# Performance work log

Measured on AMD Instinct MI355X. Metric: run time of the kernel, lower is better.

The kernel has to match this reference:

```python
import math
import jax, jax.numpy as jnp
import numpy as np

B, N_PER, FEAT, EMB, HEADS, E = 64, 512, 128, 128, 3, 131072
NEG = -1e9


def _gat(x, src, dst, emask, W, a_src, a_dst, bias):
    # PyG GATConv (concat heads, add_self_loops=True, negative_slope=0.2, eval mode -> no dropout)
    n = x.shape[0]
    H, C = a_src.shape
    h = (x @ W).reshape(n, H, C)                      # [n,H,C]
    e_src = (h * a_src[None]).sum(-1)                 # [n,H]
    e_dst = (h * a_dst[None]).sum(-1)                 # [n,H]
    loop = jnp.arange(n)
    s = jnp.concatenate([src, loop])
    d = jnp.concatenate([dst, loop])
    m = jnp.concatenate([emask, jnp.ones((n,), dtype=bool)])
    logit = jax.nn.leaky_relu(e_src[s] + e_dst[d], negative_slope=0.2)  # [E+n,H]
    logit = jnp.where(m[:, None], logit, NEG)
    mx = jax.ops.segment_max(logit, d, num_segments=n)
    ex = jnp.exp(logit - mx[d]) * m[:, None].astype(logit.dtype)
    den = jax.ops.segment_sum(ex, d, num_segments=n)
    alpha = ex / (den[d] + 1e-16)                     # edge-softmax over incoming edges
    out = jax.ops.segment_sum(alpha[:, :, None] * h[s], d, num_segments=n)
    return out.reshape(n, H * C) + bias


def _topk_pool(x, src, dst, emask, ratio, w):
    # PyG TopKPooling: score = tanh(x.w/||w||), keep ceil(ratio*n) per graph, gate kept x by score
    n = x.shape[0]
    per = n // B
    score = jnp.tanh((x @ w) / jnp.linalg.norm(w))    # [n]
    k = int(math.ceil(ratio * per))
    _, idx = jax.lax.top_k(score.reshape(B, per), k)  # [B,k]
    perm = (idx + (jnp.arange(B) * per)[:, None]).reshape(-1)
    xn = x[perm] * score[perm][:, None]
    newid = jnp.full((n,), -1, dtype=jnp.int32).at[perm].set(jnp.arange(B * k, dtype=jnp.int32))
    ns, nd = newid[src], newid[dst]
    valid = emask & (ns >= 0) & (nd >= 0)
    src = jnp.where(valid, ns, 0)
    dst = jnp.where(valid, nd, 0)
    batch = jnp.repeat(jnp.arange(B, dtype=jnp.int32), k)
    return xn, src, dst, valid, batch


def _gpool(x, batch):
    # cat([global_max_pool, global_mean_pool])
    mx = jax.ops.segment_max(x, batch, num_segments=B)
    sm = jax.ops.segment_sum(x, batch, num_segments=B)
    cnt = jax.ops.segment_sum(jnp.ones((x.shape[0], 1), x.dtype), batch, num_segments=B)
    return jnp.concatenate([mx, sm / cnt], axis=1)


def _forward(x, edge_attr, edge_index, batch_index, params):
    (W1, as1, ad1, b1, Wh1, bh1, pw1,
     W2, as2, ad2, b2, Wh2, bh2, pw2,
     W3, as3, ad3, b3, Wh3, bh3, pw3,
     Wl1, bl1, Wl2, bl2) = params
    src, dst = edge_index[0], edge_index[1]
    emask = jnp.ones((src.shape[0],), dtype=bool)

    h = _gat(x, src, dst, emask, W1, as1, ad1, b1)
    h = jax.nn.relu(h @ Wh1 + bh1)
    h, src, dst, emask, batch = _topk_pool(h, src, dst, emask, 0.8, pw1)
    x1 = _gpool(h, batch)

    h = _gat(h, src, dst, emask, W2, as2, ad2, b2)
    h = jax.nn.relu(h @ Wh2 + bh2)
    h, src, dst, emask, batch = _topk_pool(h, src, dst, emask, 0.5, pw2)
    x2 = _gpool(h, batch)

    h = _gat(h, src, dst, emask, W3, as3, ad3, b3)
    h = jax.nn.relu(h @ Wh3 + bh3)
    h, src, dst, emask, batch = _topk_pool(h, src, dst, emask, 0.2, pw3)
    x3 = _gpool(h, batch)

    z = x1 + x2 + x3
    z = jax.nn.relu(z @ Wl1 + bl1)
    # F.dropout p=0.8 skipped (eval mode)
    return z @ Wl2 + bl2


def setup_inputs() -> dict:
    key = jax.random.key(0)
    ks = jax.random.split(key, 32)
    e_per = E // B
    e = jax.random.randint(ks[0], (2, B, e_per), 0, N_PER) + (jnp.arange(B) * N_PER)[None, :, None]
    edge_index = e.reshape(2, E).astype(jnp.int32)
    inp = {
        'x': jax.random.normal(ks[1], (B * N_PER, FEAT), dtype=jnp.float32),
        'edge_attr': jnp.zeros((E, 1), dtype=jnp.float32),
        'edge_index': edge_index,
        'batch_index': jnp.repeat(jnp.arange(B, dtype=jnp.int32), N_PER),
    }
    def rn(k, shape, s=0.1):
        return jax.random.normal(k, shape, dtype=jnp.float32) * s
    names = ['W1','as1','ad1','b1','Wh1','bh1','pw1',
             'W2','as2','ad2','b2','Wh2','bh2','pw2',
             'W3','as3','ad3','b3','Wh3','bh3','pw3',
             'Wl1','bl1','Wl2','bl2']
    shapes = [(FEAT, HEADS*EMB), (HEADS, EMB), (HEADS, EMB), (HEADS*EMB,), (HEADS*EMB, EMB), (EMB,), (EMB,),
              (EMB, HEADS*EMB), (HEADS, EMB), (HEADS, EMB), (HEADS*EMB,), (HEADS*EMB, EMB), (EMB,), (EMB,),
              (EMB, HEADS*EMB), (HEADS, EMB), (HEADS, EMB), (HEADS*EMB,), (HEADS*EMB, EMB), (EMB,), (EMB,),
              (2*EMB, 512), (512,), (512, 256), (256,)]
    for i, (nm, sh) in enumerate(zip(names, shapes)):
        inp[nm] = rn(ks[2 + i], sh)
    return inp


def reference(x, edge_attr, edge_index, batch_index,
              W1, as1, ad1, b1, Wh1, bh1, pw1,
              W2, as2, ad2, b2, Wh2, bh2, pw2,
              W3, as3, ad3, b3, Wh3, bh3, pw3,
              Wl1, bl1, Wl2, bl2):
    params = (W1, as1, ad1, b1, Wh1, bh1, pw1,
              W2, as2, ad2, b2, Wh2, bh2, pw2,
              W3, as3, ad3, b3, Wh3, bh3, pw3,
              Wl1, bl1, Wl2, bl2)
    return _forward(x, edge_attr, edge_index, batch_index, params)
```

## Files before the change

### kernel.cpp

```cpp
#include <hip/hip_runtime.h>
#include <cfloat>

static __device__ __forceinline__ float lrelu(float v) { return v >= 0.f ? v : 0.2f * v; }

typedef __attribute__((ext_vector_type(8))) short bf16x8;
typedef __attribute__((ext_vector_type(8))) unsigned short ushort8;
typedef __attribute__((ext_vector_type(4))) float f32x4;

__device__ __forceinline__ unsigned short f2bf(float x) {
    unsigned u = __float_as_uint(x);
    u += 0x7FFF + ((u >> 16) & 1);
    return (unsigned short)(u >> 16);
}
__device__ __forceinline__ float bf2f(unsigned short h) {
    return __uint_as_float(((unsigned)h) << 16);
}

struct SegT { const float* s; unsigned short* dh; unsigned short* dl; int rows, cols, tr; };
struct Segs { SegT seg[7]; int cum[8]; };

__global__ __launch_bounds__(256) void split_k(Segs S, int total)
{
    int idx = blockIdx.x * 256 + threadIdx.x;
    if (idx >= total) return;
    int si = 0;
    while (idx >= S.cum[si + 1]) si++;
    int o = idx - S.cum[si];
    SegT g = S.seg[si];
    float v = g.s[o];
    unsigned short h = f2bf(v);
    unsigned short l = f2bf(v - bf2f(h));
    int di = o;
    if (g.tr) { int r = o / g.cols, c = o - r * g.cols; di = c * g.rows + r; }
    g.dh[di] = h;
    g.dl[di] = l;
}

struct WaArgs { const float* W[3]; const float* as_[3]; const float* ad_[3]; const float* pw[3]; };

__global__ __launch_bounds__(256) void wa_k(WaArgs a, float* __restrict__ wab, float* __restrict__ rn)
{
    int wid = blockIdx.x * 4 + (threadIdx.x >> 6);
    int lane = threadIdx.x & 63;
    if (wid < 2304) {
        int l = wid / 768, r = wid - l * 768;
        int j = r >> 7, kk = r & 127;
        int hh = j % 3;
        const float* av = (j < 3 ? a.as_[l] : a.ad_[l]) + hh * 128;
        const float* Wp = a.W[l] + (size_t)kk * 384 + hh * 128;
        float p = Wp[lane] * av[lane] + Wp[lane + 64] * av[lane + 64];
#pragma unroll
        for (int o = 32; o > 0; o >>= 1) p += __shfl_down(p, o);
        if (lane == 0) wab[l * 768 + j * 128 + kk] = p;
    } else if (wid < 2307) {
        int l = wid - 2304;
        const float* pw = a.pw[l];
        float v0 = pw[lane], v1 = pw[lane + 64];
        float p = v0 * v0 + v1 * v1;
#pragma unroll
        for (int o = 32; o > 0; o >>= 1) p += __shfl_down(p, o);
        if (lane == 0) rn[l] = 1.f / sqrtf(p);
    }
}

__global__ __launch_bounds__(256) void esd_k(const float* __restrict__ X,
                                             const float* __restrict__ wab,
                                             float* __restrict__ es, float* __restrict__ ed, int n)
{
    int wid = (int)((blockIdx.x * 256 + threadIdx.x) >> 6);
    int lane = threadIdx.x & 63;
    if (wid >= n) return;
    const float* xp = X + (size_t)wid * 128;
    float x0 = xp[lane], x1 = xp[lane + 64];
    float p[6];
#pragma unroll
    for (int j = 0; j < 6; j++)
        p[j] = x0 * wab[j * 128 + lane] + x1 * wab[j * 128 + 64 + lane];
#pragma unroll
    for (int o = 32; o > 0; o >>= 1)
#pragma unroll
        for (int j = 0; j < 6; j++) p[j] += __shfl_down(p[j], o);
    if (lane == 0) {
#pragma unroll
        for (int h = 0; h < 3; h++) { es[(size_t)wid * 3 + h] = p[h]; ed[(size_t)wid * 3 + h] = p[h + 3]; }
    }
}

__global__ __launch_bounds__(256) void gemm_bf2_k(const unsigned short* __restrict__ AH,
                                                  const unsigned short* __restrict__ AL,
                                                  const unsigned short* __restrict__ BTH,
                                                  const unsigned short* __restrict__ BTL,
                                                  const float* __restrict__ bias,
                                                  float* __restrict__ C,
                                                  int M, int K, int N, int relu,
                                                  const float* __restrict__ pwv,
                                                  const float* __restrict__ rnormp,
                                                  float* __restrict__ scv)
{
    __shared__ unsigned short sAH[64 * 32], sAL[64 * 32];
    __shared__ unsigned short sBH[128 * 32], sBL[128 * 32];
    __shared__ float sred[2][64];
    const int tid  = threadIdx.x;
    const int lane = tid & 63;
    const int wave = tid >> 6;
    const int wr = (wave >> 1) * 32;
    const int wc = (wave & 1) * 64;
    const int row0 = blockIdx.x * 64, col0 = blockIdx.y * 128;

    f32x4 acc[2][4];
#pragma unroll
    for (int i = 0; i < 2; i++)
#pragma unroll
        for (int j = 0; j < 4; j++) acc[i][j] = (f32x4){0.f, 0.f, 0.f, 0.f};

    const int a_r = tid >> 2;
    const int a_c = tid & 3;
    const int a_slot = a_r * 32 + ((a_c ^ ((a_r ^ (a_r >> 2)) & 3)) << 3);
    const unsigned short* ApH = AH + (size_t)(row0 + a_r) * K + a_c * 8;
    const unsigned short* ApL = AL + (size_t)(row0 + a_r) * K + a_c * 8;

    const int b_c = tid >> 1;
    const int b_h = (tid & 1) * 2;
    const int b_sw = (b_c ^ (b_c >> 2)) & 3;
    const unsigned short* BpH = BTH + (size_t)(col0 + b_c) * K + b_h * 8;
    const unsigned short* BpL = BTL + (size_t)(col0 + b_c) * K + b_h * 8;

    const int l15 = lane & 15;
    const int kc  = lane >> 4;

    for (int k0 = 0; k0 < K; k0 += 32) {
        ushort8 vah = *reinterpret_cast<const ushort8*>(ApH + k0);
        ushort8 val = *reinterpret_cast<const ushort8*>(ApL + k0);
        ushort8 vb[4];
        vb[0] = *reinterpret_cast<const ushort8*>(BpH + k0);
        vb[1] = *reinterpret_cast<const ushort8*>(BpH + k0 + 8);
        vb[2] = *reinterpret_cast<const ushort8*>(BpL + k0);
        vb[3] = *reinterpret_cast<const ushort8*>(BpL + k0 + 8);

        __syncthreads();

        *reinterpret_cast<ushort8*>(&sAH[a_slot]) = vah;
        *reinterpret_cast<ushort8*>(&sAL[a_slot]) = val;
        {
            int s0 = b_c * 32 + (((b_h + 0) ^ b_sw) << 3);
            int s1 = b_c * 32 + (((b_h + 1) ^ b_sw) << 3);
            *reinterpret_cast<ushort8*>(&sBH[s0]) = vb[0];
            *reinterpret_cast<ushort8*>(&sBH[s1]) = vb[1];
            *reinterpret_cast<ushort8*>(&sBL[s0]) = vb[2];
            *reinterpret_cast<ushort8*>(&sBL[s1]) = vb[3];
        }
        __syncthreads();

        bf16x8 aH[2], aL[2], bH[4], bL[4];
#pragma unroll
        for (int fi = 0; fi < 2; fi++) {
            int r = wr + fi * 16 + l15;
            int sidx = r * 32 + ((kc ^ ((r ^ (r >> 2)) & 3)) << 3);
            aH[fi] = *reinterpret_cast<const bf16x8*>(&sAH[sidx]);
            aL[fi] = *reinterpret_cast<const bf16x8*>(&sAL[sidx]);
        }
#pragma unroll
        for (int fj = 0; fj < 4; fj++) {
            int c = wc + fj * 16 + l15;
            int sidx = c * 32 + ((kc ^ ((c ^ (c >> 2)) & 3)) << 3);
            bH[fj] = *reinterpret_cast<const bf16x8*>(&sBH[sidx]);
            bL[fj] = *reinterpret_cast<const bf16x8*>(&sBL[sidx]);
        }
#pragma unroll
        for (int fi = 0; fi < 2; fi++)
#pragma unroll
            for (int fj = 0; fj < 4; fj++) {
                acc[fi][fj] = __builtin_amdgcn_mfma_f32_16x16x32_bf16(aH[fi], bH[fj], acc[fi][fj], 0, 0, 0);
                acc[fi][fj] = __builtin_amdgcn_mfma_f32_16x16x32_bf16(aH[fi], bL[fj], acc[fi][fj], 0, 0, 0);
                acc[fi][fj] = __builtin_amdgcn_mfma_f32_16x16x32_bf16(aL[fi], bH[fj], acc[fi][fj], 0, 0, 0);
            }
    }

    float pwl[4];
    if (scv) {
#pragma unroll
        for (int fj = 0; fj < 4; fj++) pwl[fj] = pwv[wc + fj * 16 + l15];
    }
    float pd[2][4] = {{0.f,0.f,0.f,0.f},{0.f,0.f,0.f,0.f}};
#pragma unroll
    for (int fi = 0; fi < 2; fi++) {
        int rbase = row0 + wr + fi * 16 + (lane >> 4) * 4;
#pragma unroll
        for (int q = 0; q < 4; q++) {
            int r = rbase + q;
#pragma unroll
            for (int fj = 0; fj < 4; fj++) {
                int c = col0 + wc + fj * 16 + l15;
                float v = acc[fi][fj][q];
                if (bias) v += bias[c];
                if (relu) v = fmaxf(v, 0.f);
                C[(size_t)r * N + c] = v;
                if (scv) pd[fi][q] += v * pwl[fj];
            }
        }
    }
    if (scv) {
        float rn0 = rnormp[0];
#pragma unroll
        for (int fi = 0; fi < 2; fi++)
#pragma unroll
            for (int q = 0; q < 4; q++) {
                float s = pd[fi][q];
                s += __shfl_xor(s, 1);
                s += __shfl_xor(s, 2);
                s += __shfl_xor(s, 4);
                s += __shfl_xor(s, 8);
                if (l15 == 0) sred[wc >> 6][wr + fi * 16 + (lane >> 4) * 4 + q] = s;
            }
        __syncthreads();
        if (tid < 64)
            scv[row0 + tid] = tanhf((sred[0][tid] + sred[1][tid]) * rn0);
    }
}

__global__ __launch_bounds__(256) void gemm_small_k(const float* __restrict__ A,
                                                    const float* __restrict__ B,
                                                    const float* __restrict__ bias,
                                                    float* __restrict__ C,
                                                    int M, int K, int N, int relu)
{
    int idx = blockIdx.x * 256 + threadIdx.x;
    if (idx >= M * N) return;
    int r = idx / N, c = idx - r * N;
    const float* ap = A + (size_t)r * K;
    const float* bp = B + c;
    float s = 0.f;
#pragma unroll 8
    for (int k = 0; k < K; k++) s += ap[k] * bp[(size_t)k * N];
    if (bias) s += bias[c];
    if (relu) s = fmaxf(s, 0.f);
    C[idx] = s;
}

__global__ __launch_bounds__(256) void csr_k(const int* __restrict__ src,
                                             const int* __restrict__ dst,
                                             const int* __restrict__ valid,
                                             const float* __restrict__ es,
                                             const float* __restrict__ ed,
                                             int* __restrict__ csr,
                                             int* __restrict__ beg,
                                             int* __restrict__ end,
                                             float* __restrict__ wmx,
                                             float* __restrict__ winv,
                                             float* __restrict__ wself,
                                             int per)
{
    __shared__ int sdeg[512];
    __shared__ int soff[512];
    __shared__ float ses[1536];
    __shared__ float sed[1536];
    const int g = blockIdx.x;
    const int t = threadIdx.x;
    const int bn = g * per;
    const int be = g * 2048;
    for (int i = t; i < 512; i += 256) sdeg[i] = 0;
    for (int i = t; i < per * 3; i += 256) {
        ses[i] = es[(size_t)bn * 3 + i];
        sed[i] = ed[(size_t)bn * 3 + i];
    }
    __syncthreads();
#pragma unroll
    for (int j = 0; j < 8; j++) {
        int e = be + j * 256 + t;
        if (!valid || valid[e]) atomicAdd(&sdeg[dst[e] - bn], 1);
    }
    __syncthreads();
    const int i0 = t, i1 = t + 256;
    soff[i0] = sdeg[i0]; soff[i1] = sdeg[i1];
    __syncthreads();
    for (int d = 1; d < 512; d <<= 1) {
        int a0 = (i0 >= d) ? soff[i0 - d] : 0;
        int a1 = (i1 >= d) ? soff[i1 - d] : 0;
        __syncthreads();
        soff[i0] += a0; soff[i1] += a1;
        __syncthreads();
    }
    int excl0 = 0, excl1 = 0;
    if (i0 < per) { int dg = sdeg[i0]; excl0 = soff[i0] - dg; beg[bn + i0] = be + excl0; end[bn + i0] = be + excl0 + dg; }
    if (i1 < per) { int dg = sdeg[i1]; excl1 = soff[i1] - dg; beg[bn + i1] = be + excl1; end[bn + i1] = be + excl1 + dg; }
    __syncthreads();
    if (i0 < per) { soff[i0] = excl0; sdeg[i0] = excl0; }
    if (i1 < per) { soff[i1] = excl1; sdeg[i1] = excl1; }
    __syncthreads();
#pragma unroll
    for (int j = 0; j < 8; j++) {
        int e = be + j * 256 + t;
        if (!valid || valid[e]) {
            int p = atomicAdd(&sdeg[dst[e] - bn], 1);
            csr[be + p] = e;
        }
    }
    __syncthreads();
    for (int i = t; i < per; i += 256) {
        float edv[3], m[3], den[3], selfl[3];
#pragma unroll
        for (int h = 0; h < 3; h++) {
            edv[h] = sed[i * 3 + h];
            selfl[h] = lrelu(ses[i * 3 + h] + edv[h]);
            m[h] = selfl[h];
            den[h] = 1.f;
        }
        const int pb = soff[i], pe = sdeg[i];
        for (int p = pb; p < pe; p++) {
            int e = csr[be + p];
            int sl = src[e] - bn;
#pragma unroll
            for (int h = 0; h < 3; h++) {
                float l = lrelu(ses[sl * 3 + h] + edv[h]);
                if (l <= m[h]) den[h] += __expf(l - m[h]);
                else { den[h] = den[h] * __expf(m[h] - l) + 1.f; m[h] = l; }
            }
        }
#pragma unroll
        for (int h = 0; h < 3; h++) {
            float inv = 1.f / (den[h] + 1e-16f);
            wmx[(size_t)(bn + i) * 3 + h] = m[h];
            winv[(size_t)(bn + i) * 3 + h] = inv;
            wself[(size_t)(bn + i) * 3 + h] = __expf(selfl[h] - m[h]) * inv;
        }
    }
}

__global__ __launch_bounds__(256) void agg2_k(const float* __restrict__ H,
                                              const float* __restrict__ es,
                                              const float* __restrict__ ed,
                                              const float* __restrict__ wmx,
                                              const float* __restrict__ winv,
                                              const float* __restrict__ wself,
                                              const int* __restrict__ beg,
                                              const int* __restrict__ end,
                                              const int* __restrict__ csr,
                                              const int* __restrict__ srcArr,
                                              const float* __restrict__ bias,
                                              unsigned short* __restrict__ outH,
                                              unsigned short* __restrict__ outL, int n)
{
    int nwg = gridDim.x;
    int bid = blockIdx.x;
    int swz = (bid & 7) * (nwg >> 3) + (bid >> 3);
    int wid = swz * 4 + (int)(threadIdx.x >> 6);
    int lane = threadIdx.x & 63;
    if (wid >= n) return;
    const int d = wid;
    float edv[3], mxv[3], ivv[3], wsf[3];
#pragma unroll
    for (int h = 0; h < 3; h++) {
        edv[h] = ed[(size_t)d * 3 + h];
        mxv[h] = wmx[(size_t)d * 3 + h];
        ivv[h] = winv[(size_t)d * 3 + h];
        wsf[h] = wself[(size_t)d * 3 + h];
    }
    float acc[6];
    const float* hp = H + (size_t)d * 384;
#pragma unroll
    for (int j = 0; j < 6; j++) acc[j] = wsf[j >> 1] * hp[lane + 64 * j];
    const int pb = beg[d], pe = end[d];
    for (int p = pb; p < pe; p++) {
        int eg = csr[p];
        int s = srcArr[eg];
        float w[3];
#pragma unroll
        for (int h = 0; h < 3; h++) {
            float l = lrelu(es[(size_t)s * 3 + h] + edv[h]);
            w[h] = __expf(l - mxv[h]) * ivv[h];
        }
        const float* sp = H + (size_t)s * 384;
        acc[0] += w[0] * sp[lane];
        acc[1] += w[0] * sp[lane + 64];
        acc[2] += w[1] * sp[lane + 128];
        acc[3] += w[1] * sp[lane + 192];
        acc[4] += w[2] * sp[lane + 256];
        acc[5] += w[2] * sp[lane + 320];
    }
#pragma unroll
    for (int j = 0; j < 6; j++) {
        float v = acc[j] + bias[lane + 64 * j];
        unsigned short h = f2bf(v);
        outH[(size_t)d * 384 + lane + 64 * j] = h;
        outL[(size_t)d * 384 + lane + 64 * j] = f2bf(v - bf2f(h));
    }
}

__global__ __launch_bounds__(512) void select_k(const float* __restrict__ sc,
                                                int per, int k,
                                                int* __restrict__ perm, float* __restrict__ ps,
                                                int* __restrict__ newid)
{
    __shared__ float s[512];
    __shared__ int id[512];
    const int b = blockIdx.x;
    const int t = threadIdx.x;
    const int P = blockDim.x;
    if (t < per) { s[t] = sc[(size_t)b * per + t]; id[t] = t; }
    else         { s[t] = -FLT_MAX; id[t] = per + t; }
    __syncthreads();
    for (int kk = 2; kk <= P; kk <<= 1)
        for (int j = kk >> 1; j > 0; j >>= 1) {
            int ixj = t ^ j;
            if (ixj > t) {
                float a = s[t], bq = s[ixj];
                int ia = id[t], ib = id[ixj];
                bool aBefore = (a > bq) || (a == bq && ia < ib);
                bool up = ((t & kk) == 0);
                if (up ? !aBefore : aBefore) { s[t] = bq; s[ixj] = a; id[t] = ib; id[ixj] = ia; }
            }
            __syncthreads();
        }
    if (t < k) {
        int og = b * per + id[t];
        int ng = b * k + t;
        perm[ng] = og;
        ps[ng] = s[t];
        newid[og] = ng;
    } else if (t < per) {
        newid[b * per + id[t]] = -1;
    }
}

__global__ __launch_bounds__(256) void gate_k(const float* __restrict__ H,
                                              const int* __restrict__ perm,
                                              const float* __restrict__ ps,
                                              float* __restrict__ X,
                                              unsigned short* __restrict__ XH,
                                              unsigned short* __restrict__ XL, int nNew)
{
    int wid = (int)((blockIdx.x * 256 + threadIdx.x) >> 6);
    int lane = threadIdx.x & 63;
    if (wid >= nNew) return;
    int o = perm[wid];
    float g = ps[wid];
    float v0 = H[(size_t)o * 128 + lane] * g;
    float v1 = H[(size_t)o * 128 + 64 + lane] * g;
    X[(size_t)wid * 128 + lane] = v0;
    X[(size_t)wid * 128 + 64 + lane] = v1;
    unsigned short h0 = f2bf(v0), h1 = f2bf(v1);
    XH[(size_t)wid * 128 + lane] = h0;
    XH[(size_t)wid * 128 + 64 + lane] = h1;
    XL[(size_t)wid * 128 + lane] = f2bf(v0 - bf2f(h0));
    XL[(size_t)wid * 128 + 64 + lane] = f2bf(v1 - bf2f(h1));
}

__global__ __launch_bounds__(256) void remap_k(const int* __restrict__ s_old,
                                               const int* __restrict__ d_old,
                                               const int* __restrict__ v_old,
                                               const int* __restrict__ newid,
                                               int* __restrict__ s_new, int* __restrict__ d_new,
                                               int* __restrict__ v_new, int E)
{
    int e = blockIdx.x * 256 + threadIdx.x;
    if (e >= E) return;
    int v = v_old ? v_old[e] : 1;
    int ns = -1, nd = -1;
    if (v) { ns = newid[s_old[e]]; nd = newid[d_old[e]]; }
    int ok = (v && ns >= 0 && nd >= 0) ? 1 : 0;
    s_new[e] = ok ? ns : 0;
    d_new[e] = ok ? nd : 0;
    v_new[e] = ok;
}

__global__ __launch_bounds__(1024) void gpool_k(const float* __restrict__ X,
                                                float* __restrict__ z, int k, int first)
{
    __shared__ float smx[8][128];
    __shared__ float ssm[8][128];
    const int b = blockIdx.x;
    const int col = threadIdx.x & 127;
    const int rg = threadIdx.x >> 7;
    const float* xp = X + (size_t)b * k * 128 + col;
    float mx = -FLT_MAX, sm = 0.f;
    int r = rg;
#pragma unroll 4
    for (; r + 32 <= k; r += 32) {
        float v0 = xp[(size_t)(r + 0)  * 128];
        float v1 = xp[(size_t)(r + 8)  * 128];
        float v2 = xp[(size_t)(r + 16) * 128];
        float v3 = xp[(size_t)(r + 24) * 128];
        mx = fmaxf(fmaxf(fmaxf(mx, v0), fmaxf(v1, v2)), v3);
        sm += v0 + v1 + v2 + v3;
    }
    for (; r < k; r += 8) {
        float v = xp[(size_t)r * 128];
        mx = fmaxf(mx, v);
        sm += v;
    }
    smx[rg][col] = mx;
    ssm[rg][col] = sm;
    __syncthreads();
    if (rg == 0) {
#pragma unroll
        for (int i = 1; i < 8; i++) { mx = fmaxf(mx, smx[i][col]); sm += ssm[i][col]; }
        if (first) {
            z[b * 256 + col] = mx;
            z[b * 256 + 128 + col] = sm / (float)k;
        } else {
            z[b * 256 + col] += mx;
            z[b * 256 + 128 + col] += sm / (float)k;
        }
    }
}

extern "C" void kernel_launch(void* const* d_in, const int* in_sizes, int n_in,
                              void* d_out, int out_size, void* d_ws, size_t ws_size,
                              hipStream_t stream)
{
    (void)in_sizes; (void)n_in; (void)out_size; (void)ws_size;

    const float* x   = (const float*)d_in[0];
    const int*   ei  = (const int*)d_in[2];
    const float* W1  = (const float*)d_in[4];
    const float* as1 = (const float*)d_in[5];
    const float* ad1 = (const float*)d_in[6];
    const float* b1  = (const float*)d_in[7];
    const float* Wh1 = (const float*)d_in[8];
    const float* bh1 = (const float*)d_in[9];
    const float* pw1 = (const float*)d_in[10];
    const float* W2  = (const float*)d_in[11];
    const float* as2 = (const float*)d_in[12];
    const float* ad2 = (const float*)d_in[13];
    const float* b2  = (const float*)d_in[14];
    const float* Wh2 = (const float*)d_in[15];
    const float* bh2 = (const float*)d_in[16];
    const float* pw2 = (const float*)d_in[17];
    const float* W3  = (const float*)d_in[18];
    const float* as3 = (const float*)d_in[19];
    const float* ad3 = (const float*)d_in[20];
    const float* b3  = (const float*)d_in[21];
    const float* Wh3 = (const float*)d_in[22];
    const float* bh3 = (const float*)d_in[23];
    const float* pw3 = (const float*)d_in[24];
    const float* Wl1 = (const float*)d_in[25];
    const float* bl1 = (const float*)d_in[26];
    const float* Wl2 = (const float*)d_in[27];
    const float* bl2 = (const float*)d_in[28];
    float* out = (float*)d_out;

    const int E = 131072;
    const int n1 = 32768, per1 = 512, k1 = 410;
    const int n2 = 64 * k1, per2 = k1, k2 = 205;
    const int n3 = 64 * k2, per3 = k2, k3 = 41;
    const int n4 = 64 * k3;

    char* wsb = (char*)d_ws;
    size_t off = 0;
    auto alloc = [&](size_t bytes) -> void* {
        void* p = wsb + off;
        off += (bytes + 255) & ~(size_t)255;
        return p;
    };
    float* A    = (float*)alloc((size_t)n1 * 384 * 4);
    unsigned short* BfH = (unsigned short*)alloc((size_t)n1 * 384 * 2);
    unsigned short* BfL = (unsigned short*)alloc((size_t)n1 * 384 * 2);
    unsigned short* X0H = (unsigned short*)alloc((size_t)n1 * 128 * 2);
    unsigned short* X0L = (unsigned short*)alloc((size_t)n1 * 128 * 2);
    unsigned short* XaH = (unsigned short*)alloc((size_t)n2 * 128 * 2);
    unsigned short* XaL = (unsigned short*)alloc((size_t)n2 * 128 * 2);
    unsigned short* WT[6], *WTl[6];
    for (int i = 0; i < 6; i++) {
        WT[i]  = (unsigned short*)alloc((size_t)49152 * 2);
        WTl[i] = (unsigned short*)alloc((size_t)49152 * 2);
    }
    float* ES   = (float*)alloc((size_t)n1 * 3 * 4);
    float* ED   = (float*)alloc((size_t)n1 * 3 * 4);
    float* SC   = (float*)alloc((size_t)n1 * 4);
    int*   CSR  = (int*)alloc((size_t)E * 4);
    int*   BEG  = (int*)alloc((size_t)n1 * 4);
    int*   END  = (int*)alloc((size_t)n1 * 4);
    int*   SRCA = (int*)alloc((size_t)E * 4);
    int*   DSTA = (int*)alloc((size_t)E * 4);
    int*   VALA = (int*)alloc((size_t)E * 4);
    int*   SRCB = (int*)alloc((size_t)E * 4);
    int*   DSTB = (int*)alloc((size_t)E * 4);
    int*   VALB = (int*)alloc((size_t)E * 4);
    float* X1   = (float*)alloc((size_t)n2 * 128 * 4);
    float* X2   = (float*)alloc((size_t)n3 * 128 * 4);
    float* X3   = (float*)alloc((size_t)n4 * 128 * 4);
    int*   PERM = (int*)alloc((size_t)n2 * 4);
    float* PSC  = (float*)alloc((size_t)n2 * 4);
    int*   NEWID= (int*)alloc((size_t)n1 * 4);
    float* WMX  = (float*)alloc((size_t)n1 * 3 * 4);
    float* WINV = (float*)alloc((size_t)n1 * 3 * 4);
    float* WSELF= (float*)alloc((size_t)n1 * 3 * 4);
    float* WAB  = (float*)alloc((size_t)2304 * 4);
    float* RN   = (float*)alloc((size_t)4 * 4);
    float* Z    = (float*)alloc((size_t)64 * 256 * 4);
    float* ZH   = (float*)alloc((size_t)64 * 512 * 4);

    {
        Segs S;
        const float* srcs[7] = {x, W1, Wh1, W2, Wh2, W3, Wh3};
        unsigned short* dh[7] = {X0H, WT[0], WT[1], WT[2], WT[3], WT[4], WT[5]};
        unsigned short* dl[7] = {X0L, WTl[0], WTl[1], WTl[2], WTl[3], WTl[4], WTl[5]};
        int rows[7] = {n1, 128, 384, 128, 384, 128, 384};
        int cols[7] = {128, 384, 128, 384, 128, 384, 128};
        int trs[7]  = {0, 1, 1, 1, 1, 1, 1};
        int cum = 0;
        for (int i = 0; i < 7; i++) {
            S.seg[i] = SegT{srcs[i], dh[i], dl[i], rows[i], cols[i], trs[i]};
            S.cum[i] = cum;
            cum += rows[i] * cols[i];
        }
        S.cum[7] = cum;
        split_k<<<(cum + 255) / 256, 256, 0, stream>>>(S, cum);

        WaArgs wa;
        wa.W[0] = W1;  wa.W[1] = W2;  wa.W[2] = W3;
        wa.as_[0] = as1; wa.as_[1] = as2; wa.as_[2] = as3;
        wa.ad_[0] = ad1; wa.ad_[1] = ad2; wa.ad_[2] = ad3;
        wa.pw[0] = pw1; wa.pw[1] = pw2; wa.pw[2] = pw3;
        wa_k<<<(2307 + 3) / 4, 256, 0, stream>>>(wa, WAB, RN);
    }

    auto layer = [&](const float* Xf, const unsigned short* xh, const unsigned short* xl,
                     int n, int per, int kk, int lidx,
                     const int* src, const int* dst, const int* val,
                     const unsigned short* wt, const unsigned short* wtl, const float* bb,
                     const unsigned short* wht, const unsigned short* whtl, const float* bh,
                     const float* pw,
                     float* Xn, unsigned short* XnH, unsigned short* XnL, int nNew,
                     int* srcN, int* dstN, int* valN)
    {
        esd_k<<<n / 4, 256, 0, stream>>>(Xf, WAB + lidx * 768, ES, ED, n);
        gemm_bf2_k<<<dim3(n / 64, 3), 256, 0, stream>>>(xh, xl, wt, wtl, nullptr, A, n, 128, 384, 0,
                                                        nullptr, nullptr, nullptr);
        csr_k<<<64, 256, 0, stream>>>(src, dst, val, ES, ED, CSR, BEG, END, WMX, WINV, WSELF, per);
        agg2_k<<<n / 4, 256, 0, stream>>>(A, ES, ED, WMX, WINV, WSELF, BEG, END, CSR, src, bb, BfH, BfL, n);
        gemm_bf2_k<<<dim3(n / 64, 1), 256, 0, stream>>>(BfH, BfL, wht, whtl, bh, A, n, 384, 128, 1,
                                                        pw, RN + lidx, SC);
        int P2 = 1;
        while (P2 < per) P2 <<= 1;
        select_k<<<64, P2, 0, stream>>>(SC, per, kk, PERM, PSC, NEWID);
        gate_k<<<nNew / 4, 256, 0, stream>>>(A, PERM, PSC, Xn, XnH, XnL, nNew);
        if (srcN) remap_k<<<E / 256, 256, 0, stream>>>(src, dst, val, NEWID, srcN, dstN, valN, E);
        gpool_k<<<64, 1024, 0, stream>>>(Xn, Z, kk, lidx == 0 ? 1 : 0);
    };

    layer(x,  X0H, X0L, n1, per1, k1, 0, ei,   ei + E, nullptr,
          WT[0], WTl[0], b1, WT[1], WTl[1], bh1, pw1,
          X1, XaH, XaL, n2, SRCA, DSTA, VALA);
    layer(X1, XaH, XaL, n2, per2, k2, 1, SRCA, DSTA, VALA,
          WT[2], WTl[2], b2, WT[3], WTl[3], bh2, pw2,
          X2, XaH, XaL, n3, SRCB, DSTB, VALB);
    layer(X2, XaH, XaL, n3, per3, k3, 2, SRCB, DSTB, VALB,
          WT[4], WTl[4], b3, WT[5], WTl[5], bh3, pw3,
          X3, XaH, XaL, n4, nullptr, nullptr, nullptr);

    gemm_small_k<<<(64 * 512 + 255) / 256, 256, 0, stream>>>(Z,  Wl1, bl1, ZH,  64, 256, 512, 1);
    gemm_small_k<<<(64 * 256 + 255) / 256, 256, 0, stream>>>(ZH, Wl2, bl2, out, 64, 512, 256, 0);
}
```

Baseline: 388.6 us.

## Fuse top-k selection, gating, edge remap and global pooling into one per-graph kernel

Replaces the four per-layer kernels select_k, gate_k, remap_k and gpool_k with a single pool_k launched with one 512-thread block per graph. The block sorts its graph's scores, builds the old-to-new node id map in shared memory, and uses it to remap that graph's edges. It then gathers and gates the kept rows while accumulating max/mean pooling in registers, which removes launch overhead, the global PERM/PSC/NEWID buffers and the reread of the pooled features. In exchange, the gather/gate and pooling work now runs on only 64 blocks instead of a wide grid. It also assumes each graph owns a contiguous chunk of 2048 edges whose endpoints lie inside that graph.

```diff
diff --git a/kernel.cpp b/kernel.cpp
--- a/kernel.cpp
+++ b/kernel.cpp
@@ -386,114 +386,81 @@
     }
 }
 
-__global__ __launch_bounds__(512) void select_k(const float* __restrict__ sc,
-                                                int per, int k,
-                                                int* __restrict__ perm, float* __restrict__ ps,
-                                                int* __restrict__ newid)
-{
-    __shared__ float s[512];
-    __shared__ int id[512];
+__global__ __launch_bounds__(512) void pool_k(const float* __restrict__ H,
+                                              const float* __restrict__ sc,
+                                              const int* __restrict__ s_old,
+                                              const int* __restrict__ d_old,
+                                              const int* __restrict__ v_old,
+                                              int per, int k,
+                                              float* __restrict__ X,
+                                              unsigned short* __restrict__ XH,
+                                              unsigned short* __restrict__ XL,
+                                              int* __restrict__ s_new,
+                                              int* __restrict__ d_new,
+                                              int* __restrict__ v_new,
+                                              float* __restrict__ z, int first)
+{
+    __shared__ float ss[512];
+    __shared__ int sid[512];
+    __shared__ int snew[512];
+    __shared__ float rmx[4][128];
+    __shared__ float rsm[4][128];
     const int b = blockIdx.x;
     const int t = threadIdx.x;
-    const int P = blockDim.x;
-    if (t < per) { s[t] = sc[(size_t)b * per + t]; id[t] = t; }
-    else         { s[t] = -FLT_MAX; id[t] = per + t; }
-    __syncthreads();
-    for (int kk = 2; kk <= P; kk <<= 1)
+    const int bn = b * per;
+
+    ss[t] = (t < per) ? sc[bn + t] : -FLT_MAX;
+    sid[t] = (t < per) ? t : 512 + t;
+    __syncthreads();
+    for (int kk = 2; kk <= 512; kk <<= 1)
         for (int j = kk >> 1; j > 0; j >>= 1) {
             int ixj = t ^ j;
             if (ixj > t) {
-                float a = s[t], bq = s[ixj];
-                int ia = id[t], ib = id[ixj];
+                float a = ss[t], bq = ss[ixj];
+                int ia = sid[t], ib = sid[ixj];
                 bool aBefore = (a > bq) || (a == bq && ia < ib);
                 bool up = ((t & kk) == 0);
-                if (up ? !aBefore : aBefore) { s[t] = bq; s[ixj] = a; id[t] = ib; id[ixj] = ia; }
+                if (up ? !aBefore : aBefore) { ss[t] = bq; ss[ixj] = a; sid[t] = ib; sid[ixj] = ia; }
             }
             __syncthreads();
         }
-    if (t < k) {
-        int og = b * per + id[t];
-        int ng = b * k + t;
-        perm[ng] = og;
-        ps[ng] = s[t];
-        newid[og] = ng;
-    } else if (t < per) {
-        newid[b * per + id[t]] = -1;
-    }
-}
-
-__global__ __launch_bounds__(256) void gate_k(const float* __restrict__ H,
-                                              const int* __restrict__ perm,
-                                              const float* __restrict__ ps,
-                                              float* __restrict__ X,
-                                              unsigned short* __restrict__ XH,
-                                              unsigned short* __restrict__ XL, int nNew)
-{
-    int wid = (int)((blockIdx.x * 256 + threadIdx.x) >> 6);
-    int lane = threadIdx.x & 63;
-    if (wid >= nNew) return;
-    int o = perm[wid];
-    float g = ps[wid];
-    float v0 = H[(size_t)o * 128 + lane] * g;
-    float v1 = H[(size_t)o * 128 + 64 + lane] * g;
-    X[(size_t)wid * 128 + lane] = v0;
-    X[(size_t)wid * 128 + 64 + lane] = v1;
-    unsigned short h0 = f2bf(v0), h1 = f2bf(v1);
-    XH[(size_t)wid * 128 + lane] = h0;
-    XH[(size_t)wid * 128 + 64 + lane] = h1;
-    XL[(size_t)wid * 128 + lane] = f2bf(v0 - bf2f(h0));
-    XL[(size_t)wid * 128 + 64 + lane] = f2bf(v1 - bf2f(h1));
-}
-
-__global__ __launch_bounds__(256) void remap_k(const int* __restrict__ s_old,
-                                               const int* __restrict__ d_old,
-                                               const int* __restrict__ v_old,
-                                               const int* __restrict__ newid,
-                                               int* __restrict__ s_new, int* __restrict__ d_new,
-                                               int* __restrict__ v_new, int E)
-{
-    int e = blockIdx.x * 256 + threadIdx.x;
-    if (e >= E) return;
-    int v = v_old ? v_old[e] : 1;
-    int ns = -1, nd = -1;
-    if (v) { ns = newid[s_old[e]]; nd = newid[d_old[e]]; }
-    int ok = (v && ns >= 0 && nd >= 0) ? 1 : 0;
-    s_new[e] = ok ? ns : 0;
-    d_new[e] = ok ? nd : 0;
-    v_new[e] = ok;
-}
-
-__global__ __launch_bounds__(1024) void gpool_k(const float* __restrict__ X,
-                                                float* __restrict__ z, int k, int first)
-{
-    __shared__ float smx[8][128];
-    __shared__ float ssm[8][128];
-    const int b = blockIdx.x;
-    const int col = threadIdx.x & 127;
-    const int rg = threadIdx.x >> 7;
-    const float* xp = X + (size_t)b * k * 128 + col;
+    if (sid[t] < per) snew[sid[t]] = (t < k) ? (b * k + t) : -1;
+    __syncthreads();
+
+    if (s_new) {
+        const int be = b * 2048;
+#pragma unroll
+        for (int j = 0; j < 4; j++) {
+            int e = be + j * 512 + t;
+            int v = v_old ? v_old[e] : 1;
+            int ns = -1, nd = -1;
+            if (v) { ns = snew[s_old[e] - bn]; nd = snew[d_old[e] - bn]; }
+            int ok = (v && ns >= 0 && nd >= 0) ? 1 : 0;
+            s_new[e] = ok ? ns : 0;
+            d_new[e] = ok ? nd : 0;
+            v_new[e] = ok;
+        }
+    }
+
+    const int col = t & 127, rg = t >> 7;
     float mx = -FLT_MAX, sm = 0.f;
-    int r = rg;
-#pragma unroll 4
-    for (; r + 32 <= k; r += 32) {
-        float v0 = xp[(size_t)(r + 0)  * 128];
-        float v1 = xp[(size_t)(r + 8)  * 128];
-        float v2 = xp[(size_t)(r + 16) * 128];
-        float v3 = xp[(size_t)(r + 24) * 128];
-        mx = fmaxf(fmaxf(fmaxf(mx, v0), fmaxf(v1, v2)), v3);
-        sm += v0 + v1 + v2 + v3;
-    }
-    for (; r < k; r += 8) {
-        float v = xp[(size_t)r * 128];
+    for (int i = rg; i < k; i += 4) {
+        int o = sid[i];
+        float g = ss[i];
+        float v = H[(size_t)(bn + o) * 128 + col] * g;
+        size_t di = (size_t)(b * k + i) * 128 + col;
+        X[di] = v;
+        unsigned short h = f2bf(v);
+        XH[di] = h;
+        XL[di] = f2bf(v - bf2f(h));
         mx = fmaxf(mx, v);
         sm += v;
     }
-    smx[rg][col] = mx;
-    ssm[rg][col] = sm;
+    rmx[rg][col] = mx; rsm[rg][col] = sm;
     __syncthreads();
     if (rg == 0) {
 #pragma unroll
-        for (int i = 1; i < 8; i++) { mx = fmaxf(mx, smx[i][col]); sm += ssm[i][col]; }
+        for (int i = 1; i < 4; i++) { mx = fmaxf(mx, rmx[i][col]); sm += rsm[i][col]; }
         if (first) {
             z[b * 256 + col] = mx;
             z[b * 256 + 128 + col] = sm / (float)k;
@@ -579,9 +546,6 @@
     float* X1   = (float*)alloc((size_t)n2 * 128 * 4);
     float* X2   = (float*)alloc((size_t)n3 * 128 * 4);
     float* X3   = (float*)alloc((size_t)n4 * 128 * 4);
-    int*   PERM = (int*)alloc((size_t)n2 * 4);
-    float* PSC  = (float*)alloc((size_t)n2 * 4);
-    int*   NEWID= (int*)alloc((size_t)n1 * 4);
     float* WMX  = (float*)alloc((size_t)n1 * 3 * 4);
     float* WINV = (float*)alloc((size_t)n1 * 3 * 4);
     float* WSELF= (float*)alloc((size_t)n1 * 3 * 4);
@@ -621,7 +585,7 @@
                      const unsigned short* wt, const unsigned short* wtl, const float* bb,
                      const unsigned short* wht, const unsigned short* whtl, const float* bh,
                      const float* pw,
-                     float* Xn, unsigned short* XnH, unsigned short* XnL, int nNew,
+                     float* Xn, unsigned short* XnH, unsigned short* XnL,
                      int* srcN, int* dstN, int* valN)
     {
         esd_k<<<n / 4, 256, 0, stream>>>(Xf, WAB + lidx * 768, ES, ED, n);
@@ -631,23 +595,19 @@
         agg2_k<<<n / 4, 256, 0, stream>>>(A, ES, ED, WMX, WINV, WSELF, BEG, END, CSR, src, bb, BfH, BfL, n);
         gemm_bf2_k<<<dim3(n / 64, 1), 256, 0, stream>>>(BfH, BfL, wht, whtl, bh, A, n, 384, 128, 1,
                                                         pw, RN + lidx, SC);
-        int P2 = 1;
-        while (P2 < per) P2 <<= 1;
-        select_k<<<64, P2, 0, stream>>>(SC, per, kk, PERM, PSC, NEWID);
-        gate_k<<<nNew / 4, 256, 0, stream>>>(A, PERM, PSC, Xn, XnH, XnL, nNew);
-        if (srcN) remap_k<<<E / 256, 256, 0, stream>>>(src, dst, val, NEWID, srcN, dstN, valN, E);
-        gpool_k<<<64, 1024, 0, stream>>>(Xn, Z, kk, lidx == 0 ? 1 : 0);
+        pool_k<<<64, 512, 0, stream>>>(A, SC, src, dst, val, per, kk,
+                                       Xn, XnH, XnL, srcN, dstN, valN, Z, lidx == 0 ? 1 : 0);
     };
 
     layer(x,  X0H, X0L, n1, per1, k1, 0, ei,   ei + E, nullptr,
           WT[0], WTl[0], b1, WT[1], WTl[1], bh1, pw1,
-          X1, XaH, XaL, n2, SRCA, DSTA, VALA);
+          X1, XaH, XaL, SRCA, DSTA, VALA);
     layer(X1, XaH, XaL, n2, per2, k2, 1, SRCA, DSTA, VALA,
           WT[2], WTl[2], b2, WT[3], WTl[3], bh2, pw2,
-          X2, XaH, XaL, n3, SRCB, DSTB, VALB);
+          X2, XaH, XaL, SRCB, DSTB, VALB);
     layer(X2, XaH, XaL, n3, per3, k3, 2, SRCB, DSTB, VALB,
           WT[4], WTl[4], b3, WT[5], WTl[5], bh3, pw3,
-          X3, XaH, XaL, n4, nullptr, nullptr, nullptr);
+          X3, XaH, XaL, nullptr, nullptr, nullptr);
 
     gemm_small_k<<<(64 * 512 + 255) / 256, 256, 0, stream>>>(Z,  Wl1, bl1, ZH,  64, 256, 512, 1);
     gemm_small_k<<<(64 * 256 + 255) / 256, 256, 0, stream>>>(ZH, Wl2, bl2, out, 64, 512, 256, 0);
```

Result: slower. 424.9 us (+9.3%).
